# Optimization experiments

Measured on AMD Instinct MI355X. Metric: run time of the kernel, lower is better.

## Reference

```python
import jax, jax.numpy as jnp
import numpy as np

B, S, D, H = 2, 2048, 1024, 16
DH = D // H  # 64


def setup_inputs() -> dict:
    key = jax.random.key(0)
    ks = jax.random.split(key, 12)
    scale = 0.02
    q = jax.random.normal(ks[0], (B, S, D), dtype=jnp.float32)
    k = jax.random.normal(ks[1], (B, S, D), dtype=jnp.float32)
    v = jax.random.normal(ks[2], (B, S, D), dtype=jnp.float32)
    # CTRL-style causal mask: 1.0 above the diagonal (positions to mask), 0.0 elsewhere
    mask = jnp.triu(jnp.ones((S, S), dtype=jnp.float32), k=1)
    Wq = jax.random.normal(ks[3], (D, D), dtype=jnp.float32) * scale
    bq = jnp.zeros((D,), dtype=jnp.float32)
    Wk = jax.random.normal(ks[4], (D, D), dtype=jnp.float32) * scale
    bk = jnp.zeros((D,), dtype=jnp.float32)
    Wv = jax.random.normal(ks[5], (D, D), dtype=jnp.float32) * scale
    bv = jnp.zeros((D,), dtype=jnp.float32)
    Wo = jax.random.normal(ks[6], (D, D), dtype=jnp.float32) * scale
    bo = jnp.zeros((D,), dtype=jnp.float32)
    return {"q": q, "k": k, "v": v, "mask": mask,
            "Wq": Wq, "bq": bq, "Wk": Wk, "bk": bk,
            "Wv": Wv, "bv": bv, "Wo": Wo, "bo": bo}


def _split_heads(x):
    # [B, S, D] -> [B, H, S, DH]
    b, s, _ = x.shape
    return x.reshape(b, s, H, DH).transpose(0, 2, 1, 3)


def reference(q, k, v, mask, Wq, bq, Wk, bk, Wv, bv, Wo, bo):
    # QKV projections
    qh = _split_heads(q @ Wq + bq)  # [B, H, S, DH]
    kh = _split_heads(k @ Wk + bk)
    vh = _split_heads(v @ Wv + bv)
    # scaled dot-product attention with CTRL mask convention (mask * -1e4 added)
    scores = jnp.einsum('bhqd,bhkd->bhqk', qh, kh) / jnp.sqrt(jnp.float32(DH))
    scores = scores + mask * -10000.0  # mask broadcasts [S,S] -> [B,H,S,S]
    weights = jax.nn.softmax(scores, axis=-1)
    ctx = jnp.einsum('bhqk,bhkd->bhqd', weights, vh)  # [B, H, S, DH]
    ctx = ctx.transpose(0, 2, 1, 3).reshape(q.shape[0], -1, D)  # [B, S, D]
    return ctx @ Wo + bo
```

## Files before the change

### kernel.cpp

```cpp
#include <hip/hip_runtime.h>
#include <stdint.h>

typedef unsigned short u16;
typedef __attribute__((ext_vector_type(8))) short bf16x8;
typedef __attribute__((ext_vector_type(4))) float f32x4;
typedef __attribute__((ext_vector_type(4))) unsigned short u16x4;

#define C_SCALE 0.1803368801111204f
#define C_MASK  -14426.950408889634f

__device__ __forceinline__ float bf2f(u16 x) {
  union { uint32_t u; float f; } v; v.u = ((uint32_t)x) << 16; return v.f;
}
__device__ __forceinline__ u16 f2bf(float f) {
  union { float f; uint32_t u; } v; v.f = f;
  return (u16)((v.u + 0x7FFFu + ((v.u >> 16) & 1u)) >> 16);
}

__device__ __forceinline__ void load_lds16(const void* g, void* l) {
  __builtin_amdgcn_global_load_lds(
      (const __attribute__((address_space(1))) uint32_t*)g,
      (__attribute__((address_space(3))) uint32_t*)l, 16, 0, 0);
}

__device__ __forceinline__ uint32_t pack_trunc(uint32_t f_even, uint32_t f_odd) {
  return __builtin_amdgcn_perm(f_odd, f_even, 0x07060302u);
}

__device__ __forceinline__ uint32_t cvtpk_bf16(float lo, float hi) {
  uint32_t r;
  asm("v_cvt_pk_bf16_f32 %0, %1, %2" : "=v"(r) : "v"(lo), "v"(hi));
  return r;
}

__device__ __forceinline__ bool detect_bf16(const u16* __restrict__ q) {
  int lane = threadIdx.x & 63;
  u16 w = q[lane * 4];
  int e = (w >> 7) & 0xFF;
  unsigned long long b = __ballot(e >= 96 && e <= 159);
  return __popcll(b) >= 48;
}

__global__ __launch_bounds__(256) void prep_all(const u16* __restrict__ W0,
                                                const u16* __restrict__ W1,
                                                const u16* __restrict__ W2,
                                                const u16* __restrict__ W3,
                                                u16* __restrict__ WTb,
                                                const u16* __restrict__ q,
                                                const u16* __restrict__ k,
                                                const u16* __restrict__ v,
                                                u16* __restrict__ Acast,
                                                int docast) {
  constexpr int D = 1024;
  const int z = blockIdx.z;
  const bool isbf = detect_bf16(q);

  if (z >= 4) {
    if (!docast || isbf) return;
    const int zi = z - 4;
    const u16* src = zi == 0 ? q : (zi == 1 ? k : v);
    const uint32_t* S = (const uint32_t*)src;
    u16* dst = Acast + (size_t)zi * 4 * 1024 * 1024;
    const int fb = blockIdx.y * 16 + blockIdx.x;
    const int t = threadIdx.x;
#pragma unroll
    for (int it = 0; it < 8; ++it) {
      size_t base = (size_t)fb * 16384 + it * 2048 + t * 8;
      uint4 a = *(const uint4*)&S[base];
      uint4 b = *(const uint4*)&S[base + 4];
      uint4 o;
      o.x = pack_trunc(a.x, a.y); o.y = pack_trunc(a.z, a.w);
      o.z = pack_trunc(b.x, b.y); o.w = pack_trunc(b.z, b.w);
      *(uint4*)&dst[base] = o;
    }
    return;
  }

  __shared__ u16 tile[64][72];
  const u16* W = z == 0 ? W0 : (z == 1 ? W1 : (z == 2 ? W2 : W3));
  u16* WT = WTb + (size_t)z * D * D;
  const int x0 = blockIdx.x * 64, y0 = blockIdx.y * 64;
  const int t = threadIdx.x;
  const int r = t >> 3;
  const int c8 = (t & 7) << 3;
#pragma unroll
  for (int hh = 0; hh < 2; ++hh) {
    int row = r + hh * 32;
    if (isbf) {
      *(uint4*)&tile[row][c8] = *(const uint4*)&W[(size_t)(y0 + row) * D + x0 + c8];
    } else {
      const float* Wf = (const float*)W;
      float4 f0 = *(const float4*)&Wf[(size_t)(y0 + row) * D + x0 + c8];
      float4 f1 = *(const float4*)&Wf[(size_t)(y0 + row) * D + x0 + c8 + 4];
      u16 tmp[8] = {f2bf(f0.x), f2bf(f0.y), f2bf(f0.z), f2bf(f0.w),
                    f2bf(f1.x), f2bf(f1.y), f2bf(f1.z), f2bf(f1.w)};
      *(uint4*)&tile[row][c8] = *(uint4*)tmp;
    }
  }
  __syncthreads();
#pragma unroll
  for (int hh = 0; hh < 2; ++hh) {
    int row = r + hh * 32;
    u16 tmp[8];
#pragma unroll
    for (int i = 0; i < 8; ++i) tmp[i] = tile[c8 + i][row];
    *(uint4*)&WT[(size_t)(x0 + row) * D + y0 + c8] = *(uint4*)tmp;
  }
}


__device__ __forceinline__ void stage_tile32(const u16* __restrict__ src, int row0,
                                             int k0, u16* dst, int wave, int lane) {
  constexpr int K = 1024;
#pragma unroll
  for (int p = 0; p < 2; ++p) {
    int seg = wave * 2 + p;
    int r = seg * 16 + (lane >> 2);
    int c = lane & 3;
    int cg = c ^ ((r >> 1) & 3);
    load_lds16(&src[(size_t)(row0 + r) * K + k0 + cg * 8], dst + seg * 512);
  }
}

#define FRAG_READS(Ab, Bb)                                                    \
  _Pragma("unroll") for (int i = 0; i < 4; ++i) {                             \
    int r = wm + 16 * i + lr;                                                 \
    af[i] = *(const bf16x8*)&(Ab)[r * 32 + ((quad ^ ((r >> 1) & 3)) * 8)];    \
  }                                                                           \
  _Pragma("unroll") for (int jj = 0; jj < 4; ++jj) {                          \
    int r = wn + 16 * jj + lr;                                                \
    bff[jj] = *(const bf16x8*)&(Bb)[r * 32 + ((quad ^ ((r >> 1) & 3)) * 8)];  \
  }

#define MFMA16()                                                              \
  _Pragma("unroll") for (int i = 0; i < 4; ++i)                               \
  _Pragma("unroll") for (int jj = 0; jj < 4; ++jj)                            \
      acc[i][jj] = __builtin_amdgcn_mfma_f32_16x16x32_bf16(af[i], bff[jj],    \
                                                           acc[i][jj], 0, 0, 0);

__device__ __forceinline__ void kloop2_dma(const u16* __restrict__ A,
                                           const u16* __restrict__ BT,
                                           int m0, int n0, u16* As, u16* Bs,
                                           int wave, int lane, f32x4 (&acc)[4][4]) {
  const int quad = lane >> 4, lr = lane & 15;
  const int wm = (wave & 1) * 64, wn = (wave >> 1) * 64;
  auto stage = [&](int t, int buf) {
    stage_tile32(A, m0, t * 32, As + buf * 4096, wave, lane);
    stage_tile32(BT, n0, t * 32, Bs + buf * 4096, wave, lane);
  };
  stage(0, 0);
  __syncthreads();
#pragma unroll 1
  for (int j = 0; j < 16; ++j) {
    const int t0 = 2 * j;
    {
      stage(t0 + 1, 1);
      bf16x8 af[4], bff[4];
      const u16 *Ab = As, *Bb = Bs;
      FRAG_READS(Ab, Bb)
      MFMA16()
      __syncthreads();
    }
    {
      if (t0 + 2 < 32) stage(t0 + 2, 0);
      bf16x8 af[4], bff[4];
      const u16 *Ab = As + 4096, *Bb = Bs + 4096;
      FRAG_READS(Ab, Bb)
      MFMA16()
      __syncthreads();
    }
  }
}

__device__ __forceinline__ void kloop2_f32(const float* __restrict__ Af,
                                           const u16* __restrict__ BT,
                                           int m0, int n0, u16* As, u16* Bs,
                                           int tid, f32x4 (&acc)[4][4]) {
  constexpr int K = 1024;
  const int wave = tid >> 6, lane = tid & 63;
  const int quad = lane >> 4, lr = lane & 15;
  const int wm = (wave & 1) * 64, wn = (wave >> 1) * 64;
  const int ar = tid >> 1, ah = tid & 1;
  const uint32_t* Au = (const uint32_t*)Af;
  uint4 ra0[4], ra1[4];
  auto loadA = [&](int t, uint4 (&r)[4]) {
    const uint32_t* p = &Au[(size_t)(m0 + ar) * K + t * 32 + ah * 16];
    r[0] = *(const uint4*)(p + 0);
    r[1] = *(const uint4*)(p + 4);
    r[2] = *(const uint4*)(p + 8);
    r[3] = *(const uint4*)(p + 12);
  };
  auto writeA = [&](int buf, uint4 (&rr)[4]) {
    uint4 o0, o1;
    o0.x = pack_trunc(rr[0].x, rr[0].y); o0.y = pack_trunc(rr[0].z, rr[0].w);
    o0.z = pack_trunc(rr[1].x, rr[1].y); o0.w = pack_trunc(rr[1].z, rr[1].w);
    o1.x = pack_trunc(rr[2].x, rr[2].y); o1.y = pack_trunc(rr[2].z, rr[2].w);
    o1.z = pack_trunc(rr[3].x, rr[3].y); o1.w = pack_trunc(rr[3].z, rr[3].w);
    int sw = (ar >> 1) & 3;
    int c0 = (2 * ah) ^ sw, c1 = (2 * ah + 1) ^ sw;
    *(uint4*)&As[buf * 4096 + ar * 32 + c0 * 8] = o0;
    *(uint4*)&As[buf * 4096 + ar * 32 + c1 * 8] = o1;
  };
  auto stageB = [&](int t, int buf) {
    stage_tile32(BT, n0, t * 32, Bs + buf * 4096, wave, lane);
  };
  loadA(0, ra0);
  stageB(0, 0);
  loadA(1, ra1);
  writeA(0, ra0);
  __syncthreads();
#pragma unroll 1
  for (int j = 0; j < 16; ++j) {
    const int t0 = 2 * j;
    {
      stageB(t0 + 1, 1);
      writeA(1, ra1);
      if (t0 + 2 < 32) loadA(t0 + 2, ra0);
      bf16x8 af[4], bff[4];
      const u16 *Ab = As, *Bb = Bs;
      FRAG_READS(Ab, Bb)
      MFMA16()
      __syncthreads();
    }
    {
      if (t0 + 2 < 32) { stageB(t0 + 2, 0); writeA(0, ra0); }
      if (t0 + 3 < 32) loadA(t0 + 3, ra1);
      bf16x8 af[4], bff[4];
      const u16 *Ab = As + 4096, *Bb = Bs + 4096;
      FRAG_READS(Ab, Bb)
      MFMA16()
      __syncthreads();
    }
  }
}

__global__ __launch_bounds__(256, 3) void gemm_qkv_pre(
    const u16* __restrict__ q, const u16* __restrict__ k, const u16* __restrict__ v,
    const u16* __restrict__ Acast, const u16* __restrict__ WTb,
    const u16* __restrict__ b0, const u16* __restrict__ b1, const u16* __restrict__ b2,
    u16* __restrict__ Chb) {
  __shared__ u16 As[2 * 4096];
  __shared__ u16 Bs[2 * 4096];
  const int z = blockIdx.y;
  const bool isbf = detect_bf16(q);
  const u16* Araw = z == 0 ? q : (z == 1 ? k : v);
  const u16* A = isbf ? Araw : Acast + (size_t)z * 4 * 1024 * 1024;
  const u16* bias = z == 0 ? b0 : (z == 1 ? b1 : b2);
  const u16* BT = WTb + (size_t)z * 1024 * 1024;
  u16* C = Chb + (size_t)z * 4 * 1024 * 1024;
  const int tid = threadIdx.x;
  const int wave = tid >> 6, lane = tid & 63;
  const int quad = lane >> 4, lr = lane & 15;
  const int f = blockIdx.x;
  const int n0 = (f >> 5) * 128;
  const int m0 = (f & 31) * 128;
  const int wm = (wave & 1) * 64, wn = (wave >> 1) * 64;

  f32x4 acc[4][4] = {};
  kloop2_dma(A, BT, m0, n0, As, Bs, wave, lane, acc);

  const float osc = (z == 0) ? C_SCALE : 1.0f;
#pragma unroll
  for (int i = 0; i < 4; ++i) {
#pragma unroll
    for (int jj = 0; jj < 4; ++jj) {
      int n = n0 + wn + 16 * jj + lr;
      float bv = isbf ? bf2f(bias[n]) : ((const float*)bias)[n];
#pragma unroll
      for (int r = 0; r < 4; ++r) {
        int m = m0 + wm + 16 * i + quad * 4 + r;
        float val = (acc[i][jj][r] + bv) * osc;
        int b = m >> 11, s = m & 2047, h = n >> 6, dh = n & 63;
        C[((size_t)(b * 16 + h) * 2048 + s) * 64 + dh] = f2bf(val);
      }
    }
  }
}

__global__ __launch_bounds__(256, 3) void gemm_qkv_fb(
    const u16* __restrict__ A0, const u16* __restrict__ A1, const u16* __restrict__ A2,
    const u16* __restrict__ WTb,
    const u16* __restrict__ b0, const u16* __restrict__ b1, const u16* __restrict__ b2,
    u16* __restrict__ Chb) {
  __shared__ u16 As[2 * 4096];
  __shared__ u16 Bs[2 * 4096];
  const int z = blockIdx.y;
  const u16* A = z == 0 ? A0 : (z == 1 ? A1 : A2);
  const u16* bias = z == 0 ? b0 : (z == 1 ? b1 : b2);
  const u16* BT = WTb + (size_t)z * 1024 * 1024;
  u16* C = Chb + (size_t)z * 4 * 1024 * 1024;
  const bool isbf = detect_bf16(A0);
  const int tid = threadIdx.x;
  const int wave = tid >> 6, lane = tid & 63;
  const int quad = lane >> 4, lr = lane & 15;
  const int f = blockIdx.x;
  const int n0 = (f >> 5) * 128;
  const int m0 = (f & 31) * 128;
  const int wm = (wave & 1) * 64, wn = (wave >> 1) * 64;

  f32x4 acc[4][4] = {};
  if (isbf) kloop2_dma(A, BT, m0, n0, As, Bs, wave, lane, acc);
  else      kloop2_f32((const float*)A, BT, m0, n0, As, Bs, tid, acc);

  const float osc = (z == 0) ? C_SCALE : 1.0f;
#pragma unroll
  for (int i = 0; i < 4; ++i) {
#pragma unroll
    for (int jj = 0; jj < 4; ++jj) {
      int n = n0 + wn + 16 * jj + lr;
      float bv = isbf ? bf2f(bias[n]) : ((const float*)bias)[n];
#pragma unroll
      for (int r = 0; r < 4; ++r) {
        int m = m0 + wm + 16 * i + quad * 4 + r;
        float val = (acc[i][jj][r] + bv) * osc;
        int b = m >> 11, s = m & 2047, h = n >> 6, dh = n & 63;
        C[((size_t)(b * 16 + h) * 2048 + s) * 64 + dh] = f2bf(val);
      }
    }
  }
}

__global__ __launch_bounds__(256, 2) void gemm_out(const u16* __restrict__ A,
                                                   const u16* __restrict__ BT,
                                                   const u16* __restrict__ bias,
                                                   u16* __restrict__ C,
                                                   const u16* __restrict__ qprobe) {
  constexpr int N = 1024, K = 1024;
  __shared__ u16 As[2 * 2048];
  __shared__ u16 Bs[2 * 4096];
  const bool isbf = detect_bf16(qprobe);
  const int tid = threadIdx.x;
  const int wave = tid >> 6, lane = tid & 63;
  const int quad = lane >> 4, lr = lane & 15;
  const int f = blockIdx.x;
  const int n0 = (f >> 6) * 128;
  const int m0 = (f & 63) * 64;
  const int wm = (wave & 1) * 32, wn = (wave >> 1) * 64;

  auto stage = [&](int t, int buf) {
    {
      int r = wave * 16 + (lane >> 2);
      int c = lane & 3;
      int cg = c ^ ((r >> 1) & 3);
      load_lds16(&A[(size_t)(m0 + r) * K + t * 32 + cg * 8],
                 As + buf * 2048 + wave * 512);
    }
    stage_tile32(BT, n0, t * 32, Bs + buf * 4096, wave, lane);
  };

  f32x4 acc[2][4] = {};
  stage(0, 0);
  __syncthreads();
#pragma unroll 1
  for (int j = 0; j < 16; ++j) {
    const int t0 = 2 * j;
#pragma unroll
    for (int half = 0; half < 2; ++half) {
      const int t = t0 + half;
      if (t + 1 < 32) stage(t + 1, (t + 1) & 1);
      bf16x8 af[2], bff[4];
      const u16* Ab = As + (t & 1) * 2048;
      const u16* Bb = Bs + (t & 1) * 4096;
#pragma unroll
      for (int i = 0; i < 2; ++i) {
        int r = wm + 16 * i + lr;
        af[i] = *(const bf16x8*)&Ab[r * 32 + ((quad ^ ((r >> 1) & 3)) * 8)];
      }
#pragma unroll
      for (int jj = 0; jj < 4; ++jj) {
        int r = wn + 16 * jj + lr;
        bff[jj] = *(const bf16x8*)&Bb[r * 32 + ((quad ^ ((r >> 1) & 3)) * 8)];
      }
#pragma unroll
      for (int i = 0; i < 2; ++i)
#pragma unroll
        for (int jj = 0; jj < 4; ++jj)
          acc[i][jj] =
              __builtin_amdgcn_mfma_f32_16x16x32_bf16(af[i], bff[jj], acc[i][jj], 0, 0, 0);
      __syncthreads();
    }
  }

#pragma unroll
  for (int i = 0; i < 2; ++i) {
#pragma unroll
    for (int jj = 0; jj < 4; ++jj) {
      int n = n0 + wn + 16 * jj + lr;
      float bv = isbf ? bf2f(bias[n]) : ((const float*)bias)[n];
#pragma unroll
      for (int r = 0; r < 4; ++r) {
        int m = m0 + wm + 16 * i + quad * 4 + r;
        float val = acc[i][jj][r] + bv;
        size_t idx = (size_t)m * N + n;
        if (isbf) C[idx] = f2bf(val);
        else ((float*)C)[idx] = val;
      }
    }
  }
}

__global__ __launch_bounds__(256, 2) void attn_fwd(const u16* __restrict__ Qh,
                                                   const u16* __restrict__ Kh,
                                                   const u16* __restrict__ Vh,
                                                   u16* __restrict__ ctx) {
  constexpr int S = 2048, DH = 64, Dm = 1024;
  __shared__ u16 Ks[2][64 * 64];
  __shared__ u16 Vt[2][64 * 72];
  __shared__ u16 Pl[4][16 * 72];
  const int tid = threadIdx.x;
  const int wave = tid >> 6, lane = tid & 63;
  const int quad = lane >> 4, lr = lane & 15;
  const int bh = blockIdx.y;
  const int bx = (int)blockIdx.x;
  const size_t base = (size_t)bh * S * DH;
  const u16* Q = Qh + base;
  const u16* Kp = Kh + base;
  const u16* Vp = Vh + base;
  u16* Plw = Pl[wave];
  const int b = bh >> 4, h = bh & 15;

  const int vkey2 = (tid & 31) * 2, vd8 = (tid >> 5) * 8;
  uint4 va, vbr;

  auto stageK = [&](int kt, int kbuf) {
#pragma unroll
    for (int p = 0; p < 2; ++p) {
      int s = (wave * 2 + p) * 64 + lane;
      int r = s >> 3, cg = (s & 7) ^ (r & 7);
      load_lds16(&Kp[(size_t)(kt + r) * DH + cg * 8], &Ks[kbuf][(wave * 2 + p) * 512]);
    }
  };
  auto loadV = [&](int kt) {
    va  = *(const uint4*)&Vp[(size_t)(kt + vkey2) * DH + vd8];
    vbr = *(const uint4*)&Vp[(size_t)(kt + vkey2 + 1) * DH + vd8];
  };
  auto writeV = [&](int vbuf) {
    const u16* pa = (const u16*)&va;
    const u16* pb = (const u16*)&vbr;
#pragma unroll
    for (int i = 0; i < 8; ++i) {
      uint32_t pair = (uint32_t)pa[i] | ((uint32_t)pb[i] << 16);
      *(uint32_t*)&Vt[vbuf][(vd8 + i) * 72 + vkey2] = pair;
    }
  };

  int kb = 0, vb = 0;
  for (int ph = 0; ph < 2; ++ph) {
    const int qt = ph == 0 ? (31 - bx) : bx;
    const int q0 = qt * 64;
    const int nt = qt + 1;
    const int qg = q0 + wave * 16 + lr;

    bf16x8 aQ[2];
#pragma unroll
    for (int s = 0; s < 2; ++s)
      aQ[s] = *(const bf16x8*)&Q[(size_t)(q0 + wave * 16 + lr) * DH + s * 32 + quad * 8];

    f32x4 o[4] = {};
    float m_i = -1.0e5f;
    float l_i = 0.f;

    __syncthreads();
    stageK(0, kb);
    loadV(0);
    writeV(vb);
    if (nt > 1) loadV(64);

    for (int it = 0; it < nt; ++it) {
      const int kt = it * 64;
      __syncthreads();

      bf16x8 aK[4][2], bV[4][2];
#pragma unroll
      for (int t = 0; t < 4; ++t) {
        int r = t * 16 + lr;
#pragma unroll
        for (int s = 0; s < 2; ++s) {
          int ch = (s * 4 + quad) ^ (r & 7);
          aK[t][s] = *(const bf16x8*)&Ks[kb][r * 64 + ch * 8];
        }
      }
#pragma unroll
      for (int c = 0; c < 4; ++c)
#pragma unroll
        for (int s = 0; s < 2; ++s)
          bV[c][s] = *(const bf16x8*)&Vt[vb][(c * 16 + lr) * 72 + s * 32 + quad * 8];

      if (it + 1 < nt) {
        stageK(kt + 64, kb ^ 1);
        writeV(vb ^ 1);
        if (it + 2 < nt) loadV(kt + 128);
      }

      f32x4 sc[4];
#pragma unroll
      for (int t = 0; t < 4; ++t) {
        f32x4 zz = {0.f, 0.f, 0.f, 0.f};
        zz = __builtin_amdgcn_mfma_f32_16x16x32_bf16(aK[t][0], aQ[0], zz, 0, 0, 0);
        zz = __builtin_amdgcn_mfma_f32_16x16x32_bf16(aK[t][1], aQ[1], zz, 0, 0, 0);
        sc[t] = zz;
      }

      const bool diag = (it == nt - 1);
      float v[4][4];
      float mx = -1.0e5f;
      if (diag) {
#pragma unroll
        for (int t = 0; t < 4; ++t)
#pragma unroll
          for (int r = 0; r < 4; ++r) {
            int kg = kt + t * 16 + quad * 4 + r;
            float x = sc[t][r] + ((kg > qg) ? C_MASK : 0.f);
            v[t][r] = x;
            mx = fmaxf(mx, x);
          }
      } else {
#pragma unroll
        for (int t = 0; t < 4; ++t)
#pragma unroll
          for (int r = 0; r < 4; ++r) {
            float x = sc[t][r];
            v[t][r] = x;
            mx = fmaxf(mx, x);
          }
      }
      mx = fmaxf(mx, __shfl_xor(mx, 16));
      mx = fmaxf(mx, __shfl_xor(mx, 32));

      const bool noresc = __all(mx <= m_i + 8.0f);
      const float m_new = noresc ? m_i : fmaxf(m_i, mx);

      float sum = 0.f;
      uint32_t pw[4][2];
#pragma unroll
      for (int t = 0; t < 4; ++t) {
        float p0 = exp2f(v[t][0] - m_new);
        float p1 = exp2f(v[t][1] - m_new);
        float p2 = exp2f(v[t][2] - m_new);
        float p3 = exp2f(v[t][3] - m_new);
        sum += p0 + p1 + p2 + p3;
        pw[t][0] = cvtpk_bf16(p0, p1);
        pw[t][1] = cvtpk_bf16(p2, p3);
      }
      sum += __shfl_xor(sum, 16);
      sum += __shfl_xor(sum, 32);

      if (noresc) {
        l_i += sum;
      } else {
        float alpha = exp2f(m_i - m_new);
        l_i = l_i * alpha + sum;
        m_i = m_new;
#pragma unroll
        for (int r = 0; r < 4; ++r) {
          float ab = __shfl(alpha, quad * 4 + r);
#pragma unroll
          for (int c = 0; c < 4; ++c) o[c][r] *= ab;
        }
      }
#pragma unroll
      for (int t = 0; t < 4; ++t) {
        uint2 w = {pw[t][0], pw[t][1]};
        *(uint2*)&Plw[lr * 72 + t * 16 + quad * 4] = w;
      }
      asm volatile("s_waitcnt lgkmcnt(0)" ::: "memory");
      bf16x8 aP[2];
#pragma unroll
      for (int s = 0; s < 2; ++s)
        aP[s] = *(const bf16x8*)&Plw[lr * 72 + s * 32 + quad * 8];
#pragma unroll
      for (int c = 0; c < 4; ++c)
#pragma unroll
        for (int s = 0; s < 2; ++s)
          o[c] = __builtin_amdgcn_mfma_f32_16x16x32_bf16(aP[s], bV[c][s], o[c], 0, 0, 0);
      kb ^= 1; vb ^= 1;
    }

    float linv = 1.f / l_i;
#pragma unroll
    for (int r = 0; r < 4; ++r) {
      float lb = __shfl(linv, quad * 4 + r);
      int s = q0 + wave * 16 + quad * 4 + r;
      size_t orow = ((size_t)b * S + s) * Dm + h * DH;
#pragma unroll
      for (int c = 0; c < 4; ++c) ctx[orow + c * 16 + lr] = f2bf(o[c][r] * lb);
    }
  }
}

extern "C" void kernel_launch(void* const* d_in, const int* in_sizes, int n_in,
                              void* d_out, int out_size, void* d_ws, size_t ws_size,
                              hipStream_t stream) {
  const u16* q  = (const u16*)d_in[0];
  const u16* k  = (const u16*)d_in[1];
  const u16* v  = (const u16*)d_in[2];
  const u16* Wq = (const u16*)d_in[4];
  const u16* bq = (const u16*)d_in[5];
  const u16* Wk = (const u16*)d_in[6];
  const u16* bk = (const u16*)d_in[7];
  const u16* Wv = (const u16*)d_in[8];
  const u16* bv = (const u16*)d_in[9];
  const u16* Wo = (const u16*)d_in[10];
  const u16* bo = (const u16*)d_in[11];
  u16* out = (u16*)d_out;

  constexpr size_t M1 = 1024 * 1024;
  u16* ws = (u16*)d_ws;
  u16* WT  = ws;
  u16* Qh  = WT + 4 * M1;
  u16* X   = Qh + 12 * M1;
  u16* Acast = X;
  u16* ctx   = X;

  const bool docast = ws_size >= (size_t)28 * M1 * 2;

  dim3 tb(256);
  prep_all<<<dim3(16, 16, 7), tb, 0, stream>>>(Wq, Wk, Wv, Wo, WT, q, k, v,
                                               Acast, docast ? 1 : 0);
  if (docast)
    gemm_qkv_pre<<<dim3(256, 3), tb, 0, stream>>>(q, k, v, Acast, WT, bq, bk, bv, Qh);
  else
    gemm_qkv_fb<<<dim3(256, 3), tb, 0, stream>>>(q, k, v, WT, bq, bk, bv, Qh);
  attn_fwd<<<dim3(16, 32), tb, 0, stream>>>(Qh, Qh + 4 * M1, Qh + 8 * M1, ctx);
  gemm_out<<<dim3(512), tb, 0, stream>>>(ctx, WT + 3 * M1, bo, out, q);
}
```

Measured before the change: 235.4 us.

## Write V transposed from QKV GEMM and load K/V directly to registers in attention

The QKV projection epilogue now writes V in a head-major transposed layout (dh-major, sequence contiguous). The attention kernel drops LDS staging of K and V and the per-tile block barriers. Each wave instead loads K fragments and transposed V fragments straight from global memory into registers, with K double-buffered in registers via an unrolled two-stage loop. This removes LDS traffic, the in-register V transpose and the syncthreads, but each wave now issues redundant global loads of the same K/V tiles. It also makes the transposed V store in the GEMM epilogue strided.

```diff
diff --git a/kernel.cpp b/kernel.cpp
--- a/kernel.cpp
+++ b/kernel.cpp
@@ -234,6 +234,31 @@
   }
 }
 
+__device__ __forceinline__ void qkv_epilogue(int z, int n0, int m0, int wn, int wm,
+                                             int quad, int lr, const u16* bias,
+                                             bool isbf, f32x4 (&acc)[4][4],
+                                             u16* __restrict__ C) {
+  const float osc = (z == 0) ? C_SCALE : 1.0f;
+#pragma unroll
+  for (int i = 0; i < 4; ++i) {
+#pragma unroll
+    for (int jj = 0; jj < 4; ++jj) {
+      int n = n0 + wn + 16 * jj + lr;
+      float bv = isbf ? bf2f(bias[n]) : ((const float*)bias)[n];
+#pragma unroll
+      for (int r = 0; r < 4; ++r) {
+        int m = m0 + wm + 16 * i + quad * 4 + r;
+        float val = (acc[i][jj][r] + bv) * osc;
+        int b = m >> 11, s = m & 2047, h = n >> 6, dh = n & 63;
+        size_t idx;
+        if (z == 2) idx = ((size_t)(b * 16 + h) * 64 + dh) * 2048 + s;
+        else        idx = ((size_t)(b * 16 + h) * 2048 + s) * 64 + dh;
+        C[idx] = f2bf(val);
+      }
+    }
+  }
+}
+
 __global__ __launch_bounds__(256, 3) void gemm_qkv_pre(
     const u16* __restrict__ q, const u16* __restrict__ k, const u16* __restrict__ v,
     const u16* __restrict__ Acast, const u16* __restrict__ WTb,
@@ -258,23 +283,7 @@
 
   f32x4 acc[4][4] = {};
   kloop2_dma(A, BT, m0, n0, As, Bs, wave, lane, acc);
-
-  const float osc = (z == 0) ? C_SCALE : 1.0f;
-#pragma unroll
-  for (int i = 0; i < 4; ++i) {
-#pragma unroll
-    for (int jj = 0; jj < 4; ++jj) {
-      int n = n0 + wn + 16 * jj + lr;
-      float bv = isbf ? bf2f(bias[n]) : ((const float*)bias)[n];
-#pragma unroll
-      for (int r = 0; r < 4; ++r) {
-        int m = m0 + wm + 16 * i + quad * 4 + r;
-        float val = (acc[i][jj][r] + bv) * osc;
-        int b = m >> 11, s = m & 2047, h = n >> 6, dh = n & 63;
-        C[((size_t)(b * 16 + h) * 2048 + s) * 64 + dh] = f2bf(val);
-      }
-    }
-  }
+  qkv_epilogue(z, n0, m0, wn, wm, quad, lr, bias, isbf, acc, C);
 }
 
 __global__ __launch_bounds__(256, 3) void gemm_qkv_fb(
@@ -301,23 +310,7 @@
   f32x4 acc[4][4] = {};
   if (isbf) kloop2_dma(A, BT, m0, n0, As, Bs, wave, lane, acc);
   else      kloop2_f32((const float*)A, BT, m0, n0, As, Bs, tid, acc);
-
-  const float osc = (z == 0) ? C_SCALE : 1.0f;
-#pragma unroll
-  for (int i = 0; i < 4; ++i) {
-#pragma unroll
-    for (int jj = 0; jj < 4; ++jj) {
-      int n = n0 + wn + 16 * jj + lr;
-      float bv = isbf ? bf2f(bias[n]) : ((const float*)bias)[n];
-#pragma unroll
-      for (int r = 0; r < 4; ++r) {
-        int m = m0 + wm + 16 * i + quad * 4 + r;
-        float val = (acc[i][jj][r] + bv) * osc;
-        int b = m >> 11, s = m & 2047, h = n >> 6, dh = n & 63;
-        C[((size_t)(b * 16 + h) * 2048 + s) * 64 + dh] = f2bf(val);
-      }
-    }
-  }
+  qkv_epilogue(z, n0, m0, wn, wm, quad, lr, bias, isbf, acc, C);
 }
 
 __global__ __launch_bounds__(256, 2) void gemm_out(const u16* __restrict__ A,
@@ -401,50 +394,21 @@
 
 __global__ __launch_bounds__(256, 2) void attn_fwd(const u16* __restrict__ Qh,
                                                    const u16* __restrict__ Kh,
-                                                   const u16* __restrict__ Vh,
+                                                   const u16* __restrict__ VTh,
                                                    u16* __restrict__ ctx) {
   constexpr int S = 2048, DH = 64, Dm = 1024;
-  __shared__ u16 Ks[2][64 * 64];
-  __shared__ u16 Vt[2][64 * 72];
   __shared__ u16 Pl[4][16 * 72];
   const int tid = threadIdx.x;
   const int wave = tid >> 6, lane = tid & 63;
   const int quad = lane >> 4, lr = lane & 15;
   const int bh = blockIdx.y;
   const int bx = (int)blockIdx.x;
-  const size_t base = (size_t)bh * S * DH;
-  const u16* Q = Qh + base;
-  const u16* Kp = Kh + base;
-  const u16* Vp = Vh + base;
+  const u16* Q  = Qh  + (size_t)bh * S * DH;
+  const u16* Kp = Kh  + (size_t)bh * S * DH;
+  const u16* Vt = VTh + (size_t)bh * S * DH;
   u16* Plw = Pl[wave];
   const int b = bh >> 4, h = bh & 15;
 
-  const int vkey2 = (tid & 31) * 2, vd8 = (tid >> 5) * 8;
-  uint4 va, vbr;
-
-  auto stageK = [&](int kt, int kbuf) {
-#pragma unroll
-    for (int p = 0; p < 2; ++p) {
-      int s = (wave * 2 + p) * 64 + lane;
-      int r = s >> 3, cg = (s & 7) ^ (r & 7);
-      load_lds16(&Kp[(size_t)(kt + r) * DH + cg * 8], &Ks[kbuf][(wave * 2 + p) * 512]);
-    }
-  };
-  auto loadV = [&](int kt) {
-    va  = *(const uint4*)&Vp[(size_t)(kt + vkey2) * DH + vd8];
-    vbr = *(const uint4*)&Vp[(size_t)(kt + vkey2 + 1) * DH + vd8];
-  };
-  auto writeV = [&](int vbuf) {
-    const u16* pa = (const u16*)&va;
-    const u16* pb = (const u16*)&vbr;
-#pragma unroll
-    for (int i = 0; i < 8; ++i) {
-      uint32_t pair = (uint32_t)pa[i] | ((uint32_t)pb[i] << 16);
-      *(uint32_t*)&Vt[vbuf][(vd8 + i) * 72 + vkey2] = pair;
-    }
-  };
-
-  int kb = 0, vb = 0;
   for (int ph = 0; ph < 2; ++ph) {
     const int qt = ph == 0 ? (31 - bx) : bx;
     const int q0 = qt * 64;
@@ -460,38 +424,24 @@
     float m_i = -1.0e5f;
     float l_i = 0.f;
 
-    __syncthreads();
-    stageK(0, kb);
-    loadV(0);
-    writeV(vb);
-    if (nt > 1) loadV(64);
-
-    for (int it = 0; it < nt; ++it) {
-      const int kt = it * 64;
-      __syncthreads();
-
-      bf16x8 aK[4][2], bV[4][2];
-#pragma unroll
-      for (int t = 0; t < 4; ++t) {
-        int r = t * 16 + lr;
-#pragma unroll
-        for (int s = 0; s < 2; ++s) {
-          int ch = (s * 4 + quad) ^ (r & 7);
-          aK[t][s] = *(const bf16x8*)&Ks[kb][r * 64 + ch * 8];
-        }
-      }
+    bf16x8 kA[4][2], kB[4][2], vv[4][2];
+
+    auto loadK = [&](int kt, bf16x8 (&kk)[4][2]) {
+#pragma unroll
+      for (int t = 0; t < 4; ++t)
+#pragma unroll
+        for (int s = 0; s < 2; ++s)
+          kk[t][s] = *(const bf16x8*)&Kp[(size_t)(kt + t * 16 + lr) * DH + s * 32 + quad * 8];
+    };
+    auto loadVt = [&](int kt) {
 #pragma unroll
       for (int c = 0; c < 4; ++c)
 #pragma unroll
         for (int s = 0; s < 2; ++s)
-          bV[c][s] = *(const bf16x8*)&Vt[vb][(c * 16 + lr) * 72 + s * 32 + quad * 8];
-
-      if (it + 1 < nt) {
-        stageK(kt + 64, kb ^ 1);
-        writeV(vb ^ 1);
-        if (it + 2 < nt) loadV(kt + 128);
-      }
-
+          vv[c][s] = *(const bf16x8*)&Vt[(size_t)(c * 16 + lr) * S + kt + s * 32 + quad * 8];
+    };
+
+    auto doTile = [&](bf16x8 (&aK)[4][2], int kt, bool diag) {
       f32x4 sc[4];
 #pragma unroll
       for (int t = 0; t < 4; ++t) {
@@ -501,7 +451,6 @@
         sc[t] = zz;
       }
 
-      const bool diag = (it == nt - 1);
       float v[4][4];
       float mx = -1.0e5f;
       if (diag) {
@@ -572,8 +521,26 @@
       for (int c = 0; c < 4; ++c)
 #pragma unroll
         for (int s = 0; s < 2; ++s)
-          o[c] = __builtin_amdgcn_mfma_f32_16x16x32_bf16(aP[s], bV[c][s], o[c], 0, 0, 0);
-      kb ^= 1; vb ^= 1;
+          o[c] = __builtin_amdgcn_mfma_f32_16x16x32_bf16(aP[s], vv[c][s], o[c], 0, 0, 0);
+    };
+
+    loadK(0, kA);
+    int it = 0;
+    for (;;) {
+      {
+        const int kt = it * 64;
+        loadVt(kt);
+        if (it + 1 < nt) loadK(kt + 64, kB);
+        doTile(kA, kt, it == nt - 1);
+      }
+      if (++it >= nt) break;
+      {
+        const int kt = it * 64;
+        loadVt(kt);
+        if (it + 1 < nt) loadK(kt + 64, kA);
+        doTile(kB, kt, it == nt - 1);
+      }
+      if (++it >= nt) break;
     }
 
     float linv = 1.f / l_i;
```

Measured after the change: 306.9 us. 1.3x slower.

## Write V transposed in QKV epilogue and stage it to LDS via DMA

Applied to the files above, without the earlier changes.

The QKV projection epilogue now writes V in a per-head transposed [dh][s] layout, so the attention kernel can stage V tiles into LDS with direct global-to-LDS loads and an XOR swizzle, as it already does for K. This removes the register round-trip and in-kernel transpose of V (global loads, pack, LDS stores) in the attention loop. The cost is strided, scattered stores of V in the GEMM epilogue, where consecutive lanes now write addresses 2048 elements apart.

```diff
diff --git a/kernel.cpp b/kernel.cpp
--- a/kernel.cpp
+++ b/kernel.cpp
@@ -234,6 +234,31 @@
   }
 }
 
+__device__ __forceinline__ void qkv_epilogue(int z, int n0, int m0, int wn, int wm,
+                                             int quad, int lr, const u16* bias,
+                                             bool isbf, f32x4 (&acc)[4][4],
+                                             u16* __restrict__ C) {
+  const float osc = (z == 0) ? C_SCALE : 1.0f;
+#pragma unroll
+  for (int i = 0; i < 4; ++i) {
+#pragma unroll
+    for (int jj = 0; jj < 4; ++jj) {
+      int n = n0 + wn + 16 * jj + lr;
+      float bv = isbf ? bf2f(bias[n]) : ((const float*)bias)[n];
+#pragma unroll
+      for (int r = 0; r < 4; ++r) {
+        int m = m0 + wm + 16 * i + quad * 4 + r;
+        float val = (acc[i][jj][r] + bv) * osc;
+        int b = m >> 11, s = m & 2047, h = n >> 6, dh = n & 63;
+        size_t idx;
+        if (z == 2) idx = ((size_t)(b * 16 + h) * 64 + dh) * 2048 + s;
+        else        idx = ((size_t)(b * 16 + h) * 2048 + s) * 64 + dh;
+        C[idx] = f2bf(val);
+      }
+    }
+  }
+}
+
 __global__ __launch_bounds__(256, 3) void gemm_qkv_pre(
     const u16* __restrict__ q, const u16* __restrict__ k, const u16* __restrict__ v,
     const u16* __restrict__ Acast, const u16* __restrict__ WTb,
@@ -258,23 +283,7 @@
 
   f32x4 acc[4][4] = {};
   kloop2_dma(A, BT, m0, n0, As, Bs, wave, lane, acc);
-
-  const float osc = (z == 0) ? C_SCALE : 1.0f;
-#pragma unroll
-  for (int i = 0; i < 4; ++i) {
-#pragma unroll
-    for (int jj = 0; jj < 4; ++jj) {
-      int n = n0 + wn + 16 * jj + lr;
-      float bv = isbf ? bf2f(bias[n]) : ((const float*)bias)[n];
-#pragma unroll
-      for (int r = 0; r < 4; ++r) {
-        int m = m0 + wm + 16 * i + quad * 4 + r;
-        float val = (acc[i][jj][r] + bv) * osc;
-        int b = m >> 11, s = m & 2047, h = n >> 6, dh = n & 63;
-        C[((size_t)(b * 16 + h) * 2048 + s) * 64 + dh] = f2bf(val);
-      }
-    }
-  }
+  qkv_epilogue(z, n0, m0, wn, wm, quad, lr, bias, isbf, acc, C);
 }
 
 __global__ __launch_bounds__(256, 3) void gemm_qkv_fb(
@@ -301,23 +310,7 @@
   f32x4 acc[4][4] = {};
   if (isbf) kloop2_dma(A, BT, m0, n0, As, Bs, wave, lane, acc);
   else      kloop2_f32((const float*)A, BT, m0, n0, As, Bs, tid, acc);
-
-  const float osc = (z == 0) ? C_SCALE : 1.0f;
-#pragma unroll
-  for (int i = 0; i < 4; ++i) {
-#pragma unroll
-    for (int jj = 0; jj < 4; ++jj) {
-      int n = n0 + wn + 16 * jj + lr;
-      float bv = isbf ? bf2f(bias[n]) : ((const float*)bias)[n];
-#pragma unroll
-      for (int r = 0; r < 4; ++r) {
-        int m = m0 + wm + 16 * i + quad * 4 + r;
-        float val = (acc[i][jj][r] + bv) * osc;
-        int b = m >> 11, s = m & 2047, h = n >> 6, dh = n & 63;
-        C[((size_t)(b * 16 + h) * 2048 + s) * 64 + dh] = f2bf(val);
-      }
-    }
-  }
+  qkv_epilogue(z, n0, m0, wn, wm, quad, lr, bias, isbf, acc, C);
 }
 
 __global__ __launch_bounds__(256, 2) void gemm_out(const u16* __restrict__ A,
@@ -401,26 +394,22 @@
 
 __global__ __launch_bounds__(256, 2) void attn_fwd(const u16* __restrict__ Qh,
                                                    const u16* __restrict__ Kh,
-                                                   const u16* __restrict__ Vh,
+                                                   const u16* __restrict__ VTh,
                                                    u16* __restrict__ ctx) {
   constexpr int S = 2048, DH = 64, Dm = 1024;
   __shared__ u16 Ks[2][64 * 64];
-  __shared__ u16 Vt[2][64 * 72];
+  __shared__ u16 Vs[2][64 * 64];
   __shared__ u16 Pl[4][16 * 72];
   const int tid = threadIdx.x;
   const int wave = tid >> 6, lane = tid & 63;
   const int quad = lane >> 4, lr = lane & 15;
   const int bh = blockIdx.y;
   const int bx = (int)blockIdx.x;
-  const size_t base = (size_t)bh * S * DH;
-  const u16* Q = Qh + base;
-  const u16* Kp = Kh + base;
-  const u16* Vp = Vh + base;
+  const u16* Q  = Qh  + (size_t)bh * S * DH;
+  const u16* Kp = Kh  + (size_t)bh * S * DH;
+  const u16* Vt = VTh + (size_t)bh * S * DH;
   u16* Plw = Pl[wave];
   const int b = bh >> 4, h = bh & 15;
-
-  const int vkey2 = (tid & 31) * 2, vd8 = (tid >> 5) * 8;
-  uint4 va, vbr;
 
   auto stageK = [&](int kt, int kbuf) {
 #pragma unroll
@@ -430,17 +419,12 @@
       load_lds16(&Kp[(size_t)(kt + r) * DH + cg * 8], &Ks[kbuf][(wave * 2 + p) * 512]);
     }
   };
-  auto loadV = [&](int kt) {
-    va  = *(const uint4*)&Vp[(size_t)(kt + vkey2) * DH + vd8];
-    vbr = *(const uint4*)&Vp[(size_t)(kt + vkey2 + 1) * DH + vd8];
-  };
-  auto writeV = [&](int vbuf) {
-    const u16* pa = (const u16*)&va;
-    const u16* pb = (const u16*)&vbr;
-#pragma unroll
-    for (int i = 0; i < 8; ++i) {
-      uint32_t pair = (uint32_t)pa[i] | ((uint32_t)pb[i] << 16);
-      *(uint32_t*)&Vt[vbuf][(vd8 + i) * 72 + vkey2] = pair;
+  auto stageV = [&](int kt, int vbuf) {
+#pragma unroll
+    for (int p = 0; p < 2; ++p) {
+      int s = (wave * 2 + p) * 64 + lane;
+      int r = s >> 3, cg = (s & 7) ^ (r & 7);
+      load_lds16(&Vt[(size_t)r * S + kt + cg * 8], &Vs[vbuf][(wave * 2 + p) * 512]);
     }
   };
 
@@ -462,9 +446,7 @@
 
     __syncthreads();
     stageK(0, kb);
-    loadV(0);
-    writeV(vb);
-    if (nt > 1) loadV(64);
+    stageV(0, vb);
 
     for (int it = 0; it < nt; ++it) {
       const int kt = it * 64;
@@ -481,15 +463,18 @@
         }
       }
 #pragma unroll
-      for (int c = 0; c < 4; ++c)
-#pragma unroll
-        for (int s = 0; s < 2; ++s)
-          bV[c][s] = *(const bf16x8*)&Vt[vb][(c * 16 + lr) * 72 + s * 32 + quad * 8];
+      for (int c = 0; c < 4; ++c) {
+        int rr = c * 16 + lr;
+#pragma unroll
+        for (int s = 0; s < 2; ++s) {
+          int ch = (s * 4 + quad) ^ (rr & 7);
+          bV[c][s] = *(const bf16x8*)&Vs[vb][rr * 64 + ch * 8];
+        }
+      }
 
       if (it + 1 < nt) {
         stageK(kt + 64, kb ^ 1);
-        writeV(vb ^ 1);
-        if (it + 2 < nt) loadV(kt + 128);
+        stageV(kt + 64, vb ^ 1);
       }
 
       f32x4 sc[4];
```

After: 233.0 us. No clear change (-1.0%).
